# Kernel tuning notes

Hardware: AMD Instinct MI355X
Metric: run time of the kernel (lower is better)

Reference implementation:

```python
import jax, jax.numpy as jnp
import numpy as np

EMB = 1024
HEADS = 16
HEAD_DIM = EMB // HEADS
SEQ = 2048
BATCH = 2
EPS = 1e-5


def gelu_tanh(x):
    # 0.5*x*(1+tanh(sqrt(2/pi)*(x+0.044715*x^3)))
    c = jnp.sqrt(jnp.asarray(2.0 / jnp.pi, x.dtype))
    return 0.5 * x * (1.0 + jnp.tanh(c * (x + 0.044715 * x * x * x)))


def layernorm(x, scale, shift):
    mean = jnp.mean(x, axis=-1, keepdims=True)
    # torch var(unbiased=True) -> ddof=1
    var = jnp.var(x, axis=-1, keepdims=True, ddof=1)
    return scale * (x - mean) / jnp.sqrt(var + EPS) + shift


def setup_inputs() -> dict:
    key = jax.random.key(0)
    ks = jax.random.split(key, 12)
    s = 0.02
    d = {
        "x": jax.random.normal(ks[0], (BATCH, SEQ, EMB), jnp.float32),
        "Wq": jax.random.normal(ks[1], (EMB, EMB), jnp.float32) * s,
        "bq": jnp.zeros((EMB,), jnp.float32),
        "Wk": jax.random.normal(ks[2], (EMB, EMB), jnp.float32) * s,
        "bk": jnp.zeros((EMB,), jnp.float32),
        "Wv": jax.random.normal(ks[3], (EMB, EMB), jnp.float32) * s,
        "bv": jnp.zeros((EMB,), jnp.float32),
        "Wo": jax.random.normal(ks[4], (EMB, EMB), jnp.float32) * s,
        "bo": jnp.zeros((EMB,), jnp.float32),
        "W1": jax.random.normal(ks[5], (EMB, 4 * EMB), jnp.float32) * s,
        "b1": jnp.zeros((4 * EMB,), jnp.float32),
        "W2": jax.random.normal(ks[6], (4 * EMB, EMB), jnp.float32) * s,
        "b2": jnp.zeros((EMB,), jnp.float32),
        "ln1_scale": jnp.ones((EMB,), jnp.float32),
        "ln1_shift": jnp.zeros((EMB,), jnp.float32),
        "ln2_scale": jnp.ones((EMB,), jnp.float32),
        "ln2_shift": jnp.zeros((EMB,), jnp.float32),
    }
    return d


def reference(x, Wq, bq, Wk, bk, Wv, bv, Wo, bo, W1, b1, W2, b2,
              ln1_scale, ln1_shift, ln2_scale, ln2_shift):
    b, n, _ = x.shape

    # --- attention sub-block (pre-norm) ---
    h = layernorm(x, ln1_scale, ln1_shift)
    q = (h @ Wq + bq).reshape(b, n, HEADS, HEAD_DIM).transpose(0, 2, 1, 3)
    k = (h @ Wk + bk).reshape(b, n, HEADS, HEAD_DIM).transpose(0, 2, 1, 3)
    v = (h @ Wv + bv).reshape(b, n, HEADS, HEAD_DIM).transpose(0, 2, 1, 3)

    # explicit O(n^2) scores, as in the source
    scores = jnp.einsum("bhqd,bhkd->bhqk", q, k)
    causal = jnp.triu(jnp.ones((n, n), bool), k=1)  # True above diagonal -> masked
    scores = jnp.where(causal, -jnp.inf, scores)
    weights = jax.nn.softmax(scores / jnp.sqrt(jnp.asarray(HEAD_DIM, x.dtype)), axis=-1)
    ctx = jnp.einsum("bhqk,bhkd->bhqd", weights, v)
    ctx = ctx.transpose(0, 2, 1, 3).reshape(b, n, EMB)
    x = x + (ctx @ Wo + bo)  # dropout is identity (rate 0 / eval)

    # --- FFN sub-block (pre-norm) ---
    h = layernorm(x, ln2_scale, ln2_shift)
    h = gelu_tanh(h @ W1 + b1)
    x = x + (h @ W2 + b2)
    return x
```

## Files before the change

### kernel.cpp

```cpp
#include <hip/hip_runtime.h>
#include <hip/hip_bf16.h>

#define EMB 1024
#define SEQ 2048
#define BATCH 2
#define HEADS 16
#define HDIM 64
#define ROWS (BATCH*SEQ)

typedef __hip_bfloat16 bf16;
typedef __bf16 bf16x8 __attribute__((ext_vector_type(8)));
typedef float f32x4 __attribute__((ext_vector_type(4)));

#define AS1 __attribute__((address_space(1)))
#define AS3 __attribute__((address_space(3)))

__device__ __forceinline__ void load_lds16(const void* g, void* l) {
    __builtin_amdgcn_global_load_lds((const AS1 void*)g, (AS3 void*)l, 16, 0, 0);
}

__device__ __forceinline__ float gelu_f(float x) {
    float y = 1.5957691216057308f * (x + 0.044715f * x * x * x);
    return x / (1.0f + __expf(-y));
}

__global__ void transpose_cast_kernel(const float* __restrict__ in, bf16* __restrict__ out,
                                      int R, int C) {
    __shared__ bf16 tile[32][33];
    int tx = threadIdx.x, ty = threadIdx.y;
    int c0 = blockIdx.x * 32, r0 = blockIdx.y * 32;
    for (int i = ty; i < 32; i += 8)
        tile[i][tx] = (bf16)in[(size_t)(r0 + i) * C + c0 + tx];
    __syncthreads();
    for (int i = ty; i < 32; i += 8)
        out[(size_t)(c0 + i) * R + r0 + tx] = tile[tx][i];
}

__global__ void transpose_cast4_kernel(const float* __restrict__ w0, const float* __restrict__ w1,
                                       const float* __restrict__ w2, const float* __restrict__ w3,
                                       bf16* __restrict__ o0, bf16* __restrict__ o1,
                                       bf16* __restrict__ o2, bf16* __restrict__ o3) {
    __shared__ bf16 tile[32][33];
    int z = blockIdx.z;
    const float* in = (z == 0) ? w0 : (z == 1) ? w1 : (z == 2) ? w2 : w3;
    bf16* out = (z == 0) ? o0 : (z == 1) ? o1 : (z == 2) ? o2 : o3;
    int tx = threadIdx.x, ty = threadIdx.y;
    int c0 = blockIdx.x * 32, r0 = blockIdx.y * 32;
    for (int i = ty; i < 32; i += 8)
        tile[i][tx] = (bf16)in[(size_t)(r0 + i) * 1024 + c0 + tx];
    __syncthreads();
    for (int i = ty; i < 32; i += 8)
        out[(size_t)(c0 + i) * 1024 + r0 + tx] = tile[tx][i];
}

__global__ void transpose_v_kernel(const bf16* __restrict__ v, bf16* __restrict__ vt) {
    __shared__ bf16 tile[32][33];
    int tx = threadIdx.x, ty = threadIdx.y;
    int bh = blockIdx.z;
    const bf16* in = v + (size_t)(bh >> 4) * SEQ * EMB + (bh & 15) * HDIM;
    bf16* out = vt + (size_t)bh * HDIM * SEQ;
    int s0 = blockIdx.x * 32, d0 = blockIdx.y * 32;
    for (int i = ty; i < 32; i += 8)
        tile[i][tx] = in[(size_t)(s0 + i) * EMB + d0 + tx];
    __syncthreads();
    for (int i = ty; i < 32; i += 8)
        out[(size_t)(d0 + i) * SEQ + s0 + tx] = tile[tx][i];
}

__global__ __launch_bounds__(256) void layernorm_kernel(const float* __restrict__ x,
                                                        bf16* __restrict__ out,
                                                        const float* __restrict__ scale,
                                                        const float* __restrict__ shift) {
    int row = blockIdx.x;
    int t = threadIdx.x;
    const float* xr = x + (size_t)row * EMB;
    float v[4];
    float s = 0.f, s2 = 0.f;
#pragma unroll
    for (int i = 0; i < 4; i++) {
        v[i] = xr[t + 256 * i];
        s += v[i];
        s2 += v[i] * v[i];
    }
#pragma unroll
    for (int off = 32; off > 0; off >>= 1) {
        s += __shfl_down(s, off);
        s2 += __shfl_down(s2, off);
    }
    __shared__ float sh[8];
    __shared__ float stats[2];
    int lane = t & 63, wid = t >> 6;
    if (lane == 0) { sh[wid] = s; sh[wid + 4] = s2; }
    __syncthreads();
    if (t == 0) {
        float ts = sh[0] + sh[1] + sh[2] + sh[3];
        float ts2 = sh[4] + sh[5] + sh[6] + sh[7];
        float mean = ts / (float)EMB;
        float var = (ts2 - (float)EMB * mean * mean) / (float)(EMB - 1);
        stats[0] = mean;
        stats[1] = rsqrtf(var + 1e-5f);
    }
    __syncthreads();
    float mean = stats[0], inv = stats[1];
#pragma unroll
    for (int i = 0; i < 4; i++) {
        int c = t + 256 * i;
        float y = (v[i] - mean) * inv * scale[c] + shift[c];
        out[(size_t)row * EMB + c] = (bf16)y;
    }
}

__device__ __forceinline__ void swz32(int id, int& bx, int& by) {
    int xcd = id & 7, m = id >> 3;
    by = xcd + 8 * (m & 3);
    bx = m >> 2;
}
__device__ __forceinline__ void swz64(int id, int& bx, int& by) {
    int xcd = id & 7, m = id >> 3;
    by = xcd + 8 * (m & 3) + 32 * (m >> 6);
    bx = (m >> 2) & 15;
}

template <int ACT, int RES, int OUTF>
__global__ __launch_bounds__(256) void gemm_kernel(const bf16* __restrict__ A,
                                                   const bf16* __restrict__ BT,
                                                   void* __restrict__ Cout,
                                                   const float* __restrict__ bias,
                                                   const float* __restrict__ res,
                                                   int M, int N, int K) {
    __shared__ __align__(16) bf16 lA[2][128 * 32];
    __shared__ __align__(16) bf16 lB[2][128 * 32];
    int tid = threadIdx.x;
    int wave = tid >> 6, lane = tid & 63;
    int bx, by;
    swz32(blockIdx.x, bx, by);
    int m0 = by * 128, n0 = bx * 128;
    int wm = (wave >> 1) * 64, wn = (wave & 1) * 64;
    f32x4 acc[4][4] = {};

    int srow = wave * 16 + (lane >> 2);
    int skc = (lane & 3) * 8;
    const bf16* Ag = A + (size_t)(m0 + srow) * K + skc;
    const bf16* Bg = BT + (size_t)(n0 + srow) * K + skc;
    size_t woff = (size_t)(wave * 16) * 32;

    const int an = lane & 15;
    const int ak = (lane >> 4) * 8;

    load_lds16(Ag, lA[0] + woff);
    load_lds16(Ag + (size_t)64 * K, lA[0] + woff + 64 * 32);
    load_lds16(Bg, lB[0] + woff);
    load_lds16(Bg + (size_t)64 * K, lB[0] + woff + 64 * 32);

    int nsteps = K >> 5;
    for (int t = 0; t < nsteps; t++) {
        int buf = t & 1;
        asm volatile("s_waitcnt vmcnt(0)" ::: "memory");
        __syncthreads();
        if (t + 1 < nsteps) {
            int k0 = (t + 1) * 32;
            load_lds16(Ag + k0, lA[buf ^ 1] + woff);
            load_lds16(Ag + (size_t)64 * K + k0, lA[buf ^ 1] + woff + 64 * 32);
            load_lds16(Bg + k0, lB[buf ^ 1] + woff);
            load_lds16(Bg + (size_t)64 * K + k0, lB[buf ^ 1] + woff + 64 * 32);
        }
        bf16x8 af[4], bfv[4];
#pragma unroll
        for (int i = 0; i < 4; i++)
            af[i] = *(const bf16x8*)(lA[buf] + (wm + 16 * i + an) * 32 + ak);
#pragma unroll
        for (int j = 0; j < 4; j++)
            bfv[j] = *(const bf16x8*)(lB[buf] + (wn + 16 * j + an) * 32 + ak);
#pragma unroll
        for (int i = 0; i < 4; i++)
#pragma unroll
            for (int j = 0; j < 4; j++)
                acc[i][j] = __builtin_amdgcn_mfma_f32_16x16x32_bf16(af[i], bfv[j], acc[i][j], 0, 0, 0);
    }
#pragma unroll
    for (int j = 0; j < 4; j++) {
        int col = n0 + wn + 16 * j + an;
        float bv = bias[col];
#pragma unroll
        for (int i = 0; i < 4; i++) {
#pragma unroll
            for (int r = 0; r < 4; r++) {
                int row = m0 + wm + 16 * i + (lane >> 4) * 4 + r;
                float vx = acc[i][j][r] + bv;
                if (ACT == 1) vx = gelu_f(vx);
                size_t idx = (size_t)row * N + col;
                if (RES == 2) vx += res[idx];
                if (OUTF == 0) ((bf16*)Cout)[idx] = (bf16)vx;
                else ((float*)Cout)[idx] = vx;
            }
        }
    }
}

template <int RES, int OUTF>
__global__ __launch_bounds__(256) void gemm64_kernel(const bf16* __restrict__ A,
                                                     const bf16* __restrict__ BT,
                                                     void* __restrict__ Cout,
                                                     const float* __restrict__ bias,
                                                     const float* __restrict__ res,
                                                     int M, int N, int K) {
    __shared__ __align__(16) bf16 lA[2][2][64 * 32];
    __shared__ __align__(16) bf16 lB[2][2][64 * 32];
    int tid = threadIdx.x;
    int wave = tid >> 6, lane = tid & 63;
    int bx, by;
    swz64(blockIdx.x, bx, by);
    int m0 = by * 64, n0 = bx * 64;
    int wm = (wave >> 1) * 32, wn = (wave & 1) * 32;
    f32x4 acc[2][2] = {};

    int srow = wave * 16 + (lane >> 2);
    int skc = (lane & 3) * 8;
    const bf16* Ag = A + (size_t)(m0 + srow) * K + skc;
    const bf16* Bg = BT + (size_t)(n0 + srow) * K + skc;
    size_t woff = (size_t)(wave * 16) * 32;

    const int an = lane & 15;
    const int ak = (lane >> 4) * 8;

    load_lds16(Ag, &lA[0][0][woff]);
    load_lds16(Ag + 32, &lA[0][1][woff]);
    load_lds16(Bg, &lB[0][0][woff]);
    load_lds16(Bg + 32, &lB[0][1][woff]);

    int nsteps = K >> 6;
    for (int t = 0; t < nsteps; t++) {
        int buf = t & 1;
        asm volatile("s_waitcnt vmcnt(0)" ::: "memory");
        __syncthreads();
        if (t + 1 < nsteps) {
            int k0 = (t + 1) * 64;
            load_lds16(Ag + k0, &lA[buf ^ 1][0][woff]);
            load_lds16(Ag + k0 + 32, &lA[buf ^ 1][1][woff]);
            load_lds16(Bg + k0, &lB[buf ^ 1][0][woff]);
            load_lds16(Bg + k0 + 32, &lB[buf ^ 1][1][woff]);
        }
#pragma unroll
        for (int h = 0; h < 2; h++) {
            bf16x8 af[2], bfv[2];
#pragma unroll
            for (int i = 0; i < 2; i++)
                af[i] = *(const bf16x8*)(&lA[buf][h][(wm + 16 * i + an) * 32 + ak]);
#pragma unroll
            for (int j = 0; j < 2; j++)
                bfv[j] = *(const bf16x8*)(&lB[buf][h][(wn + 16 * j + an) * 32 + ak]);
#pragma unroll
            for (int i = 0; i < 2; i++)
#pragma unroll
                for (int j = 0; j < 2; j++)
                    acc[i][j] = __builtin_amdgcn_mfma_f32_16x16x32_bf16(af[i], bfv[j], acc[i][j], 0, 0, 0);
        }
    }
#pragma unroll
    for (int j = 0; j < 2; j++) {
        int col = n0 + wn + 16 * j + an;
        float bv = bias[col];
#pragma unroll
        for (int i = 0; i < 2; i++) {
#pragma unroll
            for (int r = 0; r < 4; r++) {
                int row = m0 + wm + 16 * i + (lane >> 4) * 4 + r;
                float vx = acc[i][j][r] + bv;
                size_t idx = (size_t)row * N + col;
                if (RES == 2) vx += res[idx];
                if (OUTF == 0) ((bf16*)Cout)[idx] = (bf16)vx;
                else ((float*)Cout)[idx] = vx;
            }
        }
    }
}

__global__ __launch_bounds__(256) void gemm_qkv_kernel(const bf16* __restrict__ A,
                                                       const bf16* __restrict__ BT,
                                                       bf16* __restrict__ qo,
                                                       bf16* __restrict__ ko,
                                                       bf16* __restrict__ vo,
                                                       const float* __restrict__ bq,
                                                       const float* __restrict__ bk,
                                                       const float* __restrict__ bv) {
    const int K = EMB;
    __shared__ __align__(16) bf16 lA[2][128 * 32];
    __shared__ __align__(16) bf16 lB[2][128 * 32];
    int tid = threadIdx.x;
    int wave = tid >> 6, lane = tid & 63;
    int bx, by;
    swz32(blockIdx.x, bx, by);
    int m0 = by * 128, n0 = bx * 128;
    int wm = (wave >> 1) * 64, wn = (wave & 1) * 64;
    f32x4 acc[4][4] = {};

    int srow = wave * 16 + (lane >> 2);
    int skc = (lane & 3) * 8;
    const bf16* Ag = A + (size_t)(m0 + srow) * K + skc;
    const bf16* Bg = BT + (size_t)(n0 + srow) * K + skc;
    size_t woff = (size_t)(wave * 16) * 32;

    const int an = lane & 15;
    const int ak = (lane >> 4) * 8;

    load_lds16(Ag, lA[0] + woff);
    load_lds16(Ag + (size_t)64 * K, lA[0] + woff + 64 * 32);
    load_lds16(Bg, lB[0] + woff);
    load_lds16(Bg + (size_t)64 * K, lB[0] + woff + 64 * 32);

    const int nsteps = K >> 5;
    for (int t = 0; t < nsteps; t++) {
        int buf = t & 1;
        asm volatile("s_waitcnt vmcnt(0)" ::: "memory");
        __syncthreads();
        if (t + 1 < nsteps) {
            int k0 = (t + 1) * 32;
            load_lds16(Ag + k0, lA[buf ^ 1] + woff);
            load_lds16(Ag + (size_t)64 * K + k0, lA[buf ^ 1] + woff + 64 * 32);
            load_lds16(Bg + k0, lB[buf ^ 1] + woff);
            load_lds16(Bg + (size_t)64 * K + k0, lB[buf ^ 1] + woff + 64 * 32);
        }
        bf16x8 af[4], bfv[4];
#pragma unroll
        for (int i = 0; i < 4; i++)
            af[i] = *(const bf16x8*)(lA[buf] + (wm + 16 * i + an) * 32 + ak);
#pragma unroll
        for (int j = 0; j < 4; j++)
            bfv[j] = *(const bf16x8*)(lB[buf] + (wn + 16 * j + an) * 32 + ak);
#pragma unroll
        for (int i = 0; i < 4; i++)
#pragma unroll
            for (int j = 0; j < 4; j++)
                acc[i][j] = __builtin_amdgcn_mfma_f32_16x16x32_bf16(af[i], bfv[j], acc[i][j], 0, 0, 0);
    }
#pragma unroll
    for (int j = 0; j < 4; j++) {
        int col = n0 + wn + 16 * j + an;
        int region = col >> 10;
        int c = col & 1023;
        const float* bias = (region == 0) ? bq : (region == 1) ? bk : bv;
        bf16* outp = (region == 0) ? qo : (region == 1) ? ko : vo;
        float scl = (region == 0) ? 0.125f : 1.0f;
        float bvv = bias[c];
#pragma unroll
        for (int i = 0; i < 4; i++) {
#pragma unroll
            for (int r = 0; r < 4; r++) {
                int row = m0 + wm + 16 * i + (lane >> 4) * 4 + r;
                float vx = (acc[i][j][r] + bvv) * scl;
                outp[(size_t)row * EMB + c] = (bf16)vx;
            }
        }
    }
}

__global__ __launch_bounds__(256) void attn_kernel(const bf16* __restrict__ q,
                                                   const bf16* __restrict__ k,
                                                   const bf16* __restrict__ vt,
                                                   bf16* __restrict__ ctx) {
    __shared__ __align__(16) bf16 ksm[2][2048];
    __shared__ __align__(16) bf16 vsm[2][2048];
    __shared__ __align__(16) bf16 pbuf[4][16][32];
    int tid = threadIdx.x;
    int wave = tid >> 6, lane = tid & 63;
    int id = blockIdx.x;
    int bh = id >> 5;
    int bx = ((id & 31) + bh) & 31;
    int b = bh >> 4, h = bh & 15;
    int q0 = bx * 64 + wave * 16;
    const bf16* qp = q + (size_t)b * SEQ * EMB + h * HDIM;
    const bf16* kp = k + (size_t)b * SEQ * EMB + h * HDIM;
    const bf16* vp = vt + (size_t)bh * HDIM * SEQ;

    int an = lane & 15;
    int aq = lane >> 4;
    bf16x8 qf0 = *(const bf16x8*)(qp + (size_t)(q0 + an) * EMB + aq * 8);
    bf16x8 qf1 = *(const bf16x8*)(qp + (size_t)(q0 + an) * EMB + 32 + aq * 8);
    f32x4 o[4] = {};
    float lp[4] = {0.f, 0.f, 0.f, 0.f};

    const bf16* kg = kp + (size_t)((wave & 1) * 16 + (lane >> 2)) * EMB + ((wave & 2) ? 32 : 0) + (lane & 3) * 8;
    const bf16* vg = vp + (size_t)(wave * 16 + (lane >> 2)) * SEQ + (lane & 3) * 8;

    int nsteps = 2 * bx + 2;
    load_lds16(kg, (char*)ksm[0] + wave * 1024);
    load_lds16(vg, (char*)vsm[0] + wave * 1024);

    for (int t = 0; t < nsteps; t++) {
        int buf = t & 1;
        asm volatile("s_waitcnt vmcnt(0)" ::: "memory");
        __syncthreads();
        if (t + 1 < nsteps) {
            int kvn = (t + 1) * 32;
            load_lds16(kg + (size_t)kvn * EMB, (char*)ksm[buf ^ 1] + wave * 1024);
            load_lds16(vg + kvn, (char*)vsm[buf ^ 1] + wave * 1024);
        }
        const char* kb = (const char*)ksm[buf];
        bf16x8 kf0 = *(const bf16x8*)(kb + an * 64 + aq * 16);
        bf16x8 kf1 = *(const bf16x8*)(kb + 2048 + an * 64 + aq * 16);
        bf16x8 kf2 = *(const bf16x8*)(kb + (16 + an) * 64 + aq * 16);
        bf16x8 kf3 = *(const bf16x8*)(kb + 2048 + (16 + an) * 64 + aq * 16);
        f32x4 s0 = {}, s1 = {};
        s0 = __builtin_amdgcn_mfma_f32_16x16x32_bf16(qf0, kf0, s0, 0, 0, 0);
        s0 = __builtin_amdgcn_mfma_f32_16x16x32_bf16(qf1, kf1, s0, 0, 0, 0);
        s1 = __builtin_amdgcn_mfma_f32_16x16x32_bf16(qf0, kf2, s1, 0, 0, 0);
        s1 = __builtin_amdgcn_mfma_f32_16x16x32_bf16(qf1, kf3, s1, 0, 0, 0);
        int kv = t * 32;
        if (t < nsteps - 2) {
#pragma unroll
            for (int r = 0; r < 4; r++) {
                float p0 = __expf(s0[r]);
                float p1 = __expf(s1[r]);
                lp[r] += p0 + p1;
                pbuf[wave][aq * 4 + r][an] = (bf16)p0;
                pbuf[wave][aq * 4 + r][16 + an] = (bf16)p1;
            }
        } else {
#pragma unroll
            for (int r = 0; r < 4; r++) {
                int row = q0 + aq * 4 + r;
                float p0 = (kv + an > row) ? 0.f : __expf(s0[r]);
                float p1 = (kv + 16 + an > row) ? 0.f : __expf(s1[r]);
                lp[r] += p0 + p1;
                pbuf[wave][aq * 4 + r][an] = (bf16)p0;
                pbuf[wave][aq * 4 + r][16 + an] = (bf16)p1;
            }
        }
        asm volatile("s_waitcnt lgkmcnt(0)" ::: "memory");
        bf16x8 pa = *(const bf16x8*)(&pbuf[wave][an][aq * 8]);
        const char* vb = (const char*)vsm[buf];
#pragma unroll
        for (int dt = 0; dt < 4; dt++) {
            bf16x8 vf = *(const bf16x8*)(vb + (dt * 16 + an) * 64 + aq * 16);
            o[dt] = __builtin_amdgcn_mfma_f32_16x16x32_bf16(pa, vf, o[dt], 0, 0, 0);
        }
    }
#pragma unroll
    for (int r = 0; r < 4; r++) {
        float v = lp[r];
        v += __shfl_xor(v, 1);
        v += __shfl_xor(v, 2);
        v += __shfl_xor(v, 4);
        v += __shfl_xor(v, 8);
        lp[r] = v;
    }
#pragma unroll
    for (int dt = 0; dt < 4; dt++) {
#pragma unroll
        for (int r = 0; r < 4; r++) {
            int row = q0 + aq * 4 + r;
            int col = h * HDIM + dt * 16 + an;
            ctx[((size_t)b * SEQ + row) * EMB + col] = (bf16)(o[dt][r] / lp[r]);
        }
    }
}

extern "C" void kernel_launch(void* const* d_in, const int* in_sizes, int n_in,
                              void* d_out, int out_size, void* d_ws, size_t ws_size,
                              hipStream_t stream) {
    const float* x = (const float*)d_in[0];
    const float* Wq = (const float*)d_in[1];
    const float* bq = (const float*)d_in[2];
    const float* Wk = (const float*)d_in[3];
    const float* bk = (const float*)d_in[4];
    const float* Wv = (const float*)d_in[5];
    const float* bv = (const float*)d_in[6];
    const float* Wo = (const float*)d_in[7];
    const float* bo = (const float*)d_in[8];
    const float* W1 = (const float*)d_in[9];
    const float* b1 = (const float*)d_in[10];
    const float* W2 = (const float*)d_in[11];
    const float* b2 = (const float*)d_in[12];
    const float* ln1s = (const float*)d_in[13];
    const float* ln1b = (const float*)d_in[14];
    const float* ln2s = (const float*)d_in[15];
    const float* ln2b = (const float*)d_in[16];
    float* out = (float*)d_out;

    char* ws = (char*)d_ws;
    const size_t MB = 1ull << 20;
    bf16* WqT = (bf16*)(ws + 0 * MB);
    bf16* WkT = (bf16*)(ws + 2 * MB);
    bf16* WvT = (bf16*)(ws + 4 * MB);
    bf16* WoT = (bf16*)(ws + 6 * MB);
    bf16* W1T = (bf16*)(ws + 8 * MB);
    bf16* W2T = (bf16*)(ws + 16 * MB);
    bf16* hbuf = (bf16*)(ws + 24 * MB);
    bf16* qbuf = (bf16*)(ws + 32 * MB);
    bf16* kbuf = (bf16*)(ws + 40 * MB);
    bf16* vbuf = (bf16*)(ws + 48 * MB);
    bf16* vtb = (bf16*)(ws + 56 * MB);
    bf16* ctxb = (bf16*)(ws + 64 * MB);
    float* x1 = (float*)(ws + 72 * MB);
    bf16* hff = (bf16*)(ws + 32 * MB);

    dim3 tb(32, 8);
    transpose_cast4_kernel<<<dim3(32, 32, 4), tb, 0, stream>>>(Wq, Wk, Wv, Wo, WqT, WkT, WvT, WoT);
    transpose_cast_kernel<<<dim3(128, 32), tb, 0, stream>>>(W1, W1T, 1024, 4096);
    transpose_cast_kernel<<<dim3(32, 128), tb, 0, stream>>>(W2, W2T, 4096, 1024);

    layernorm_kernel<<<ROWS, 256, 0, stream>>>(x, hbuf, ln1s, ln1b);

    gemm_qkv_kernel<<<768, 256, 0, stream>>>(hbuf, WqT, qbuf, kbuf, vbuf, bq, bk, bv);

    transpose_v_kernel<<<dim3(64, 2, 32), tb, 0, stream>>>(vbuf, vtb);

    attn_kernel<<<1024, 256, 0, stream>>>(qbuf, kbuf, vtb, ctxb);

    gemm64_kernel<2, 1><<<1024, 256, 0, stream>>>(ctxb, WoT, x1, bo, x, ROWS, EMB, EMB);

    layernorm_kernel<<<ROWS, 256, 0, stream>>>(x1, hbuf, ln2s, ln2b);

    gemm_kernel<1, 0, 0><<<1024, 256, 0, stream>>>(hbuf, W1T, hff, b1, nullptr, ROWS, 4 * EMB, EMB);

    gemm64_kernel<2, 1><<<1024, 256, 0, stream>>>(hff, W2T, out, b2, x1, ROWS, EMB, 4 * EMB);
}
```

Before: 372.9 us.

## Replace 128x128 QKV and FFN1 GEMMs with 256x256 multi-buffered 8-wave kernel

Adds a gemm256 kernel with 256x256 output tiles, 512 threads, BK=64 and four LDS stages per operand. It uses an XOR-swizzled LDS layout to avoid bank conflicts and issues staged global-to-LDS prefetches interleaved with MFMA phases. The MFMA phases run under raised wave priority. This kernel replaces both the QKV projection and the FFN-up GEMM, raising arithmetic intensity and hiding load latency. The trade-off is fewer blocks: 192 and 256 blocks, which may leave CUs idle on the QKV launch. The 128KB LDS footprint also limits occupancy to one block per CU.

```diff
diff --git a/kernel.cpp b/kernel.cpp
--- a/kernel.cpp
+++ b/kernel.cpp
@@ -110,88 +110,141 @@
     }
 }
 
-__device__ __forceinline__ void swz32(int id, int& bx, int& by) {
-    int xcd = id & 7, m = id >> 3;
-    by = xcd + 8 * (m & 3);
-    bx = m >> 2;
-}
 __device__ __forceinline__ void swz64(int id, int& bx, int& by) {
     int xcd = id & 7, m = id >> 3;
     by = xcd + 8 * (m & 3) + 32 * (m >> 6);
     bx = (m >> 2) & 15;
 }
 
-template <int ACT, int RES, int OUTF>
-__global__ __launch_bounds__(256) void gemm_kernel(const bf16* __restrict__ A,
-                                                   const bf16* __restrict__ BT,
-                                                   void* __restrict__ Cout,
-                                                   const float* __restrict__ bias,
-                                                   const float* __restrict__ res,
-                                                   int M, int N, int K) {
-    __shared__ __align__(16) bf16 lA[2][128 * 32];
-    __shared__ __align__(16) bf16 lB[2][128 * 32];
-    int tid = threadIdx.x;
-    int wave = tid >> 6, lane = tid & 63;
-    int bx, by;
-    swz32(blockIdx.x, bx, by);
-    int m0 = by * 128, n0 = bx * 128;
-    int wm = (wave >> 1) * 64, wn = (wave & 1) * 64;
-    f32x4 acc[4][4] = {};
-
-    int srow = wave * 16 + (lane >> 2);
-    int skc = (lane & 3) * 8;
-    const bf16* Ag = A + (size_t)(m0 + srow) * K + skc;
-    const bf16* Bg = BT + (size_t)(n0 + srow) * K + skc;
-    size_t woff = (size_t)(wave * 16) * 32;
-
-    const int an = lane & 15;
-    const int ak = (lane >> 4) * 8;
-
-    load_lds16(Ag, lA[0] + woff);
-    load_lds16(Ag + (size_t)64 * K, lA[0] + woff + 64 * 32);
-    load_lds16(Bg, lB[0] + woff);
-    load_lds16(Bg + (size_t)64 * K, lB[0] + woff + 64 * 32);
-
-    int nsteps = K >> 5;
-    for (int t = 0; t < nsteps; t++) {
-        int buf = t & 1;
-        asm volatile("s_waitcnt vmcnt(0)" ::: "memory");
-        __syncthreads();
-        if (t + 1 < nsteps) {
-            int k0 = (t + 1) * 32;
-            load_lds16(Ag + k0, lA[buf ^ 1] + woff);
-            load_lds16(Ag + (size_t)64 * K + k0, lA[buf ^ 1] + woff + 64 * 32);
-            load_lds16(Bg + k0, lB[buf ^ 1] + woff);
-            load_lds16(Bg + (size_t)64 * K + k0, lB[buf ^ 1] + woff + 64 * 32);
-        }
-        bf16x8 af[4], bfv[4];
-#pragma unroll
-        for (int i = 0; i < 4; i++)
-            af[i] = *(const bf16x8*)(lA[buf] + (wm + 16 * i + an) * 32 + ak);
-#pragma unroll
-        for (int j = 0; j < 4; j++)
-            bfv[j] = *(const bf16x8*)(lB[buf] + (wn + 16 * j + an) * 32 + ak);
-#pragma unroll
-        for (int i = 0; i < 4; i++)
-#pragma unroll
-            for (int j = 0; j < 4; j++)
-                acc[i][j] = __builtin_amdgcn_mfma_f32_16x16x32_bf16(af[i], bfv[j], acc[i][j], 0, 0, 0);
-    }
-#pragma unroll
-    for (int j = 0; j < 4; j++) {
-        int col = n0 + wn + 16 * j + an;
-        float bv = bias[col];
-#pragma unroll
-        for (int i = 0; i < 4; i++) {
-#pragma unroll
-            for (int r = 0; r < 4; r++) {
-                int row = m0 + wm + 16 * i + (lane >> 4) * 4 + r;
-                float vx = acc[i][j][r] + bv;
-                if (ACT == 1) vx = gelu_f(vx);
-                size_t idx = (size_t)row * N + col;
-                if (RES == 2) vx += res[idx];
-                if (OUTF == 0) ((bf16*)Cout)[idx] = (bf16)vx;
-                else ((float*)Cout)[idx] = vx;
+__device__ __forceinline__ void stage_half(const bf16* g, bf16* lds, int tid, size_t rowK64) {
+    load_lds16(g, lds + tid * 8);
+    load_lds16(g + rowK64, lds + 4096 + tid * 8);
+}
+
+template <int ACT, int QKV>
+__global__ __launch_bounds__(512, 2) void gemm256_kernel(
+    const bf16* __restrict__ A, const bf16* __restrict__ BT,
+    bf16* __restrict__ C0, bf16* __restrict__ C1, bf16* __restrict__ C2,
+    const float* __restrict__ bias0, const float* __restrict__ bias1,
+    const float* __restrict__ bias2, int N, int K) {
+    __shared__ __align__(16) bf16 lA[4][128 * 64];
+    __shared__ __align__(16) bf16 lB[4][128 * 64];
+    const int tid = threadIdx.x;
+    const int wave = tid >> 6, lane = tid & 63;
+    const int an = lane & 15, aq = lane >> 4;
+    const int wr = wave >> 2, wc = wave & 3;
+
+    int id = blockIdx.x;
+    int xcd = id & 7, m = id >> 3;
+    int by = xcd * 2 + (m & 1);
+    int bx = m >> 1;
+    int m0 = by * 256, n0 = bx * 256;
+
+    const int srow = tid >> 3;
+    const int csw = ((tid & 7) ^ (srow & 7)) * 8;
+    const bf16* Ag = A + (size_t)(m0 + srow) * K + csw;
+    const bf16* Bg = BT + (size_t)(n0 + srow) * K + csw;
+    const size_t rowK64 = (size_t)64 * K;
+    const size_t rowK128 = (size_t)128 * K;
+
+    stage_half(Bg, lB[0], tid, rowK64);
+    stage_half(Bg + rowK128, lB[1], tid, rowK64);
+    stage_half(Ag, lA[0], tid, rowK64);
+    stage_half(Ag + rowK128, lA[1], tid, rowK64);
+    stage_half(Bg + 64, lB[2], tid, rowK64);
+    stage_half(Bg + rowK128 + 64, lB[3], tid, rowK64);
+    asm volatile("s_waitcnt vmcnt(4)" ::: "memory");
+    __builtin_amdgcn_s_barrier();
+
+    f32x4 acc[8][4] = {};
+    const int NT = K >> 6;
+    const int lrB = (wc & 1) * 64;
+
+    for (int t = 0; t < NT; ++t) {
+        const bf16* As = lA[(2 * t + wr) & 3];
+        const bf16* Bs = lB[(2 * t + (wc >> 1)) & 3];
+        bf16x8 bfv[4][2];
+#pragma unroll
+        for (int p = 0; p < 4; ++p) {
+            bf16x8 af[2][2];
+            if (p == 0) {
+#pragma unroll
+                for (int j = 0; j < 4; ++j)
+#pragma unroll
+                    for (int kk = 0; kk < 2; ++kk) {
+                        int r = lrB + 16 * j + an;
+                        bfv[j][kk] = *(const bf16x8*)(Bs + r * 64 + ((kk * 4 + aq) ^ (r & 7)) * 8);
+                    }
+            }
+#pragma unroll
+            for (int ii = 0; ii < 2; ++ii)
+#pragma unroll
+                for (int kk = 0; kk < 2; ++kk) {
+                    int r = 16 * (2 * p + ii) + an;
+                    af[ii][kk] = *(const bf16x8*)(As + r * 64 + ((kk * 4 + aq) ^ (r & 7)) * 8);
+                }
+            if (p == 0) {
+                if (t + 1 < NT)
+                    stage_half(Ag + (size_t)(t + 1) * 64, lA[(2 * t + 2) & 3], tid, rowK64);
+            } else if (p == 1) {
+                if (t + 1 < NT)
+                    stage_half(Ag + rowK128 + (size_t)(t + 1) * 64, lA[(2 * t + 3) & 3], tid, rowK64);
+            } else if (p == 2) {
+                if (t + 2 < NT)
+                    stage_half(Bg + (size_t)(t + 2) * 64, lB[(2 * t + 4) & 3], tid, rowK64);
+            } else {
+                if (t + 2 < NT) {
+                    stage_half(Bg + rowK128 + (size_t)(t + 2) * 64, lB[(2 * t + 5) & 3], tid, rowK64);
+                    asm volatile("s_waitcnt vmcnt(4)" ::: "memory");
+                } else {
+                    asm volatile("s_waitcnt vmcnt(0)" ::: "memory");
+                }
+            }
+            __builtin_amdgcn_s_barrier();
+            asm volatile("s_waitcnt lgkmcnt(0)" ::: "memory");
+            __builtin_amdgcn_s_setprio(1);
+#pragma unroll
+            for (int ii = 0; ii < 2; ++ii)
+#pragma unroll
+                for (int j = 0; j < 4; ++j)
+#pragma unroll
+                    for (int kk = 0; kk < 2; ++kk)
+                        acc[2 * p + ii][j] = __builtin_amdgcn_mfma_f32_16x16x32_bf16(
+                            af[ii][kk], bfv[j][kk], acc[2 * p + ii][j], 0, 0, 0);
+            __builtin_amdgcn_s_setprio(0);
+            __builtin_amdgcn_s_barrier();
+        }
+    }
+
+#pragma unroll
+    for (int j = 0; j < 4; ++j) {
+        int col = n0 + wc * 64 + 16 * j + an;
+        if (QKV == 0) {
+            float bv = bias0[col];
+#pragma unroll
+            for (int i = 0; i < 8; ++i) {
+#pragma unroll
+                for (int r = 0; r < 4; ++r) {
+                    int row = m0 + wr * 128 + 16 * i + aq * 4 + r;
+                    float v = acc[i][j][r] + bv;
+                    if (ACT == 1) v = gelu_f(v);
+                    C0[(size_t)row * N + col] = (bf16)v;
+                }
+            }
+        } else {
+            int region = col >> 10, c = col & 1023;
+            const float* bp = (region == 0) ? bias0 : (region == 1) ? bias1 : bias2;
+            bf16* outp = (region == 0) ? C0 : (region == 1) ? C1 : C2;
+            float scl = (region == 0) ? 0.125f : 1.0f;
+            float bv = bp[c];
+#pragma unroll
+            for (int i = 0; i < 8; ++i) {
+#pragma unroll
+                for (int r = 0; r < 4; ++r) {
+                    int row = m0 + wr * 128 + 16 * i + aq * 4 + r;
+                    float v = (acc[i][j][r] + bv) * scl;
+                    outp[(size_t)row * EMB + c] = (bf16)v;
+                }
             }
         }
     }
@@ -270,85 +323,6 @@
                 if (RES == 2) vx += res[idx];
                 if (OUTF == 0) ((bf16*)Cout)[idx] = (bf16)vx;
                 else ((float*)Cout)[idx] = vx;
-            }
-        }
-    }
-}
-
-__global__ __launch_bounds__(256) void gemm_qkv_kernel(const bf16* __restrict__ A,
-                                                       const bf16* __restrict__ BT,
-                                                       bf16* __restrict__ qo,
-                                                       bf16* __restrict__ ko,
-                                                       bf16* __restrict__ vo,
-                                                       const float* __restrict__ bq,
-                                                       const float* __restrict__ bk,
-                                                       const float* __restrict__ bv) {
-    const int K = EMB;
-    __shared__ __align__(16) bf16 lA[2][128 * 32];
-    __shared__ __align__(16) bf16 lB[2][128 * 32];
-    int tid = threadIdx.x;
-    int wave = tid >> 6, lane = tid & 63;
-    int bx, by;
-    swz32(blockIdx.x, bx, by);
-    int m0 = by * 128, n0 = bx * 128;
-    int wm = (wave >> 1) * 64, wn = (wave & 1) * 64;
-    f32x4 acc[4][4] = {};
-
-    int srow = wave * 16 + (lane >> 2);
-    int skc = (lane & 3) * 8;
-    const bf16* Ag = A + (size_t)(m0 + srow) * K + skc;
-    const bf16* Bg = BT + (size_t)(n0 + srow) * K + skc;
-    size_t woff = (size_t)(wave * 16) * 32;
-
-    const int an = lane & 15;
-    const int ak = (lane >> 4) * 8;
-
-    load_lds16(Ag, lA[0] + woff);
-    load_lds16(Ag + (size_t)64 * K, lA[0] + woff + 64 * 32);
-    load_lds16(Bg, lB[0] + woff);
-    load_lds16(Bg + (size_t)64 * K, lB[0] + woff + 64 * 32);
-
-    const int nsteps = K >> 5;
-    for (int t = 0; t < nsteps; t++) {
-        int buf = t & 1;
-        asm volatile("s_waitcnt vmcnt(0)" ::: "memory");
-        __syncthreads();
-        if (t + 1 < nsteps) {
-            int k0 = (t + 1) * 32;
-            load_lds16(Ag + k0, lA[buf ^ 1] + woff);
-            load_lds16(Ag + (size_t)64 * K + k0, lA[buf ^ 1] + woff + 64 * 32);
-            load_lds16(Bg + k0, lB[buf ^ 1] + woff);
-            load_lds16(Bg + (size_t)64 * K + k0, lB[buf ^ 1] + woff + 64 * 32);
-        }
-        bf16x8 af[4], bfv[4];
-#pragma unroll
-        for (int i = 0; i < 4; i++)
-            af[i] = *(const bf16x8*)(lA[buf] + (wm + 16 * i + an) * 32 + ak);
-#pragma unroll
-        for (int j = 0; j < 4; j++)
-            bfv[j] = *(const bf16x8*)(lB[buf] + (wn + 16 * j + an) * 32 + ak);
-#pragma unroll
-        for (int i = 0; i < 4; i++)
-#pragma unroll
-            for (int j = 0; j < 4; j++)
-                acc[i][j] = __builtin_amdgcn_mfma_f32_16x16x32_bf16(af[i], bfv[j], acc[i][j], 0, 0, 0);
-    }
-#pragma unroll
-    for (int j = 0; j < 4; j++) {
-        int col = n0 + wn + 16 * j + an;
-        int region = col >> 10;
-        int c = col & 1023;
-        const float* bias = (region == 0) ? bq : (region == 1) ? bk : bv;
-        bf16* outp = (region == 0) ? qo : (region == 1) ? ko : vo;
-        float scl = (region == 0) ? 0.125f : 1.0f;
-        float bvv = bias[c];
-#pragma unroll
-        for (int i = 0; i < 4; i++) {
-#pragma unroll
-            for (int r = 0; r < 4; r++) {
-                int row = m0 + wm + 16 * i + (lane >> 4) * 4 + r;
-                float vx = (acc[i][j][r] + bvv) * scl;
-                outp[(size_t)row * EMB + c] = (bf16)vx;
             }
         }
     }
@@ -501,7 +475,8 @@
 
     layernorm_kernel<<<ROWS, 256, 0, stream>>>(x, hbuf, ln1s, ln1b);
 
-    gemm_qkv_kernel<<<768, 256, 0, stream>>>(hbuf, WqT, qbuf, kbuf, vbuf, bq, bk, bv);
+    gemm256_kernel<0, 1><<<192, 512, 0, stream>>>(hbuf, WqT, qbuf, kbuf, vbuf,
+                                                  bq, bk, bv, EMB, EMB);
 
     transpose_v_kernel<<<dim3(64, 2, 32), tb, 0, stream>>>(vbuf, vtb);
 
@@ -511,7 +486,8 @@
 
     layernorm_kernel<<<ROWS, 256, 0, stream>>>(x1, hbuf, ln2s, ln2b);
 
-    gemm_kernel<1, 0, 0><<<1024, 256, 0, stream>>>(hbuf, W1T, hff, b1, nullptr, ROWS, 4 * EMB, EMB);
+    gemm256_kernel<1, 0><<<256, 512, 0, stream>>>(hbuf, W1T, hff, nullptr, nullptr,
+                                                  b1, nullptr, nullptr, 4 * EMB, EMB);
 
     gemm64_kernel<2, 1><<<1024, 256, 0, stream>>>(hff, W2T, out, b2, x1, ROWS, EMB, 4 * EMB);
 }
```

Result: no change. 367.4 us (-1.5%).
